# Optimization experiments

Measured on AMD Instinct MI355X. Metric: run time of the kernel, lower is better.

Reference implementation:

```python
import jax, jax.numpy as jnp
import numpy as np

TEMPERATURE = 0.01
STRIDE = 16  # original image coords -> feature grid (1024 / 64)


def setup_inputs() -> dict:
    key = jax.random.key(0)
    k1, k2, k3, k4, k5 = jax.random.split(key, 5)
    B, C, Hf, Wf, N = 32, 256, 64, 64, 64
    feats_src = jax.random.normal(k1, (B, C, Hf, Wf), dtype=jnp.float32)
    feats_trg = jax.random.normal(k2, (B, C, Hf, Wf), dtype=jnp.float32)
    # keypoints in original-image coordinates [0, 1024)
    kps_src = jax.random.uniform(k3, (B, N, 2), dtype=jnp.float32) * 1024.0
    kps_trg = jax.random.uniform(k4, (B, N, 2), dtype=jnp.float32) * 1024.0
    kps_mask = jax.random.bernoulli(k5, 0.7, (B, N))
    return {"feats_src": feats_src, "feats_trg": feats_trg,
            "kps_src": kps_src, "kps_trg": kps_trg, "kps_mask": kps_mask}


def _l2_normalize(x):
    # F.normalize(x, dim=1): x / max(||x||_2, eps)
    n = jnp.linalg.norm(x, axis=1, keepdims=True)
    return x / jnp.maximum(n, 1e-12)


def _kps_to_flat_idx(kps, Hf, Wf):
    # int(coord/16) truncation (coords >= 0 so trunc == floor), then clamp.
    fx = jnp.clip((kps[..., 0] / STRIDE).astype(jnp.int32), 0, Wf - 1)
    fy = jnp.clip((kps[..., 1] / STRIDE).astype(jnp.int32), 0, Hf - 1)
    return fy * Wf + fx  # (B, N)


def reference(feats_src, feats_trg, kps_src, kps_trg, kps_mask):
    B, C, Hf, Wf = feats_src.shape
    fs = _l2_normalize(feats_src).reshape(B, C, Hf * Wf)
    ft = _l2_normalize(feats_trg).reshape(B, C, Hf * Wf)

    src_idx = _kps_to_flat_idx(kps_src, Hf, Wf)  # (B, N)
    trg_idx = _kps_to_flat_idx(kps_trg, Hf, Wf)  # (B, N)

    # Gather query vectors at source keypoint cells: (B, C, N)
    queries = jnp.take_along_axis(fs, src_idx[:, None, :], axis=2)
    # Batched logits over all target cells: (B, N, Hf*Wf)
    logits = jnp.einsum('bcn,bcm->bnm', queries, ft) / TEMPERATURE

    logp = jax.nn.log_softmax(logits, axis=-1)
    nll = -jnp.take_along_axis(logp, trg_idx[..., None], axis=-1)[..., 0]  # (B, N)

    m = kps_mask.astype(nll.dtype)
    count = jnp.sum(m)
    # Masked mean over valid keypoints; 0 if no valid keypoints (matches torch).
    return jnp.sum(nll * m) / jnp.maximum(count, 1.0)
```

## Files before the change

### kernel.cpp

```cpp
#include <hip/hip_runtime.h>
#include <hip/hip_fp16.h>
#include <cstdint>

#define BB 32
#define CC 256
#define HF 64
#define WF 64
#define MM 4096
#define NN 64
#define MCHUNKS 32
#define MPB 128
#define KSTEPS 8

typedef _Float16 half8 __attribute__((ext_vector_type(8)));
typedef __fp16 fp16x2 __attribute__((ext_vector_type(2)));
typedef float f32x4 __attribute__((ext_vector_type(4)));


__global__ void phase0_gather_norm(const float* __restrict__ fs,
                                   const float* __restrict__ kps_src,
                                   const float* __restrict__ kps_trg,
                                   _Float16* __restrict__ wq,
                                   int* __restrict__ trgidx) {
  int blk = blockIdx.x;
  int b = blk >> 6, n = blk & 63;
  int c = threadIdx.x;

  float kx = kps_src[blk * 2 + 0];
  float ky = kps_src[blk * 2 + 1];
  int fx = min(max((int)(kx * (1.0f / 16.0f)), 0), WF - 1);
  int fy = min(max((int)(ky * (1.0f / 16.0f)), 0), HF - 1);
  int pix = fy * WF + fx;

  float x = fs[((size_t)b * CC + c) * MM + pix];

  float v = x * x;
  #pragma unroll
  for (int off = 32; off >= 1; off >>= 1) v += __shfl_xor(v, off);
  __shared__ float ssum[4];
  int wid = c >> 6, lane = c & 63;
  if (lane == 0) ssum[wid] = v;
  __syncthreads();
  float tot = ssum[0] + ssum[1] + ssum[2] + ssum[3];
  float inv = 1.0f / fmaxf(sqrtf(tot), 1e-12f);

  int ks = c >> 5, kg = (c >> 3) & 3, j = c & 7;
  int nt = n >> 4, nr = n & 15;
  int lane_f = kg * 16 + nr;
  size_t off = (size_t)b * 16384 + (size_t)((ks * 4 + nt) * 64 + lane_f) * 8 + j;
  wq[off] = (_Float16)(x * inv);

  if (c == 0) {
    float tx = kps_trg[blk * 2 + 0], ty = kps_trg[blk * 2 + 1];
    int gx = min(max((int)(tx * (1.0f / 16.0f)), 0), WF - 1);
    int gy = min(max((int)(ty * (1.0f / 16.0f)), 0), HF - 1);
    trgidx[blk] = gy * WF + gx;
  }
}

__global__ void __launch_bounds__(256, 4)
phaseB(const float* __restrict__ ft,
       const _Float16* __restrict__ wq,
       const int* __restrict__ tidx,
       float* __restrict__ part,
       float* __restrict__ trgl) {
  __shared__ _Float16 qf[16384];
  __shared__ int trg_lds[NN];
  __shared__ float pM[4 * NN], pS[4 * NN];

  int b = blockIdx.x >> 5, mc = blockIdx.x & 31;
  int tid = threadIdx.x;

  const uint4* src = (const uint4*)(wq + (size_t)b * 16384);
  uint4* dst = (uint4*)qf;
  #pragma unroll
  for (int i = 0; i < 8; ++i) dst[tid + 256 * i] = src[tid + 256 * i];
  if (tid < NN) trg_lds[tid] = tidx[b * NN + tid];
  __syncthreads();

  int w = tid >> 6, lane = tid & 63, g = lane >> 4, col = lane & 15;
  int m0 = mc * MPB + w * 32;
  const float* fb = ft + (size_t)b * CC * MM;
  const float* lb0 = fb + (size_t)(g * 8) * MM + (m0 + col);
  const float* lb1 = lb0 + 16;

  f32x4 acc[4][2];
  #pragma unroll
  for (int nt = 0; nt < 4; ++nt)
    #pragma unroll
    for (int mt = 0; mt < 2; ++mt) acc[nt][mt] = (f32x4){0.f, 0.f, 0.f, 0.f};
  float ss0 = 0.f, ss1 = 0.f;

  const half8* qv = (const half8*)qf;

  float cur0[8], cur1[8], nxt0[8], nxt1[8];
  #pragma unroll
  for (int j = 0; j < 8; ++j) {
    cur0[j] = lb0[(size_t)j * MM];
    cur1[j] = lb1[(size_t)j * MM];
  }

  #pragma unroll
  for (int ks = 0; ks < KSTEPS; ++ks) {
    if (ks + 1 < KSTEPS) {
      #pragma unroll
      for (int j = 0; j < 8; ++j) {
        nxt0[j] = lb0[(size_t)((ks + 1) * 32 + j) * MM];
        nxt1[j] = lb1[(size_t)((ks + 1) * 32 + j) * MM];
      }
    }

    half8 a0 = qv[(ks * 4 + 0) * 64 + lane];
    half8 a1 = qv[(ks * 4 + 1) * 64 + lane];
    half8 a2 = qv[(ks * 4 + 2) * 64 + lane];
    half8 a3 = qv[(ks * 4 + 3) * 64 + lane];

    half8 b0, b1;
    #pragma unroll
    for (int j = 0; j < 4; ++j) {
      ss0 += cur0[2 * j] * cur0[2 * j] + cur0[2 * j + 1] * cur0[2 * j + 1];
      ss1 += cur1[2 * j] * cur1[2 * j] + cur1[2 * j + 1] * cur1[2 * j + 1];
      fp16x2 h0 = __builtin_amdgcn_cvt_pkrtz(cur0[2 * j], cur0[2 * j + 1]);
      fp16x2 h1 = __builtin_amdgcn_cvt_pkrtz(cur1[2 * j], cur1[2 * j + 1]);
      b0[2 * j] = (_Float16)h0[0]; b0[2 * j + 1] = (_Float16)h0[1];
      b1[2 * j] = (_Float16)h1[0]; b1[2 * j + 1] = (_Float16)h1[1];
    }

    acc[0][0] = __builtin_amdgcn_mfma_f32_16x16x32_f16(a0, b0, acc[0][0], 0, 0, 0);
    acc[1][0] = __builtin_amdgcn_mfma_f32_16x16x32_f16(a1, b0, acc[1][0], 0, 0, 0);
    acc[2][0] = __builtin_amdgcn_mfma_f32_16x16x32_f16(a2, b0, acc[2][0], 0, 0, 0);
    acc[3][0] = __builtin_amdgcn_mfma_f32_16x16x32_f16(a3, b0, acc[3][0], 0, 0, 0);
    acc[0][1] = __builtin_amdgcn_mfma_f32_16x16x32_f16(a0, b1, acc[0][1], 0, 0, 0);
    acc[1][1] = __builtin_amdgcn_mfma_f32_16x16x32_f16(a1, b1, acc[1][1], 0, 0, 0);
    acc[2][1] = __builtin_amdgcn_mfma_f32_16x16x32_f16(a2, b1, acc[2][1], 0, 0, 0);
    acc[3][1] = __builtin_amdgcn_mfma_f32_16x16x32_f16(a3, b1, acc[3][1], 0, 0, 0);

    #pragma unroll
    for (int j = 0; j < 8; ++j) { cur0[j] = nxt0[j]; cur1[j] = nxt1[j]; }
  }

  ss0 += __shfl_xor(ss0, 16); ss0 += __shfl_xor(ss0, 32);
  ss1 += __shfl_xor(ss1, 16); ss1 += __shfl_xor(ss1, 32);
  float scale0 = 100.0f / fmaxf(sqrtf(ss0), 1e-12f);
  float scale1 = 100.0f / fmaxf(sqrtf(ss1), 1e-12f);

  int mA = m0 + col, mB = m0 + 16 + col;

  #pragma unroll
  for (int nt = 0; nt < 4; ++nt) {
    #pragma unroll
    for (int r = 0; r < 4; ++r) {
      int n = nt * 16 + g * 4 + r;
      float v0 = acc[nt][0][r] * scale0;
      float v1 = acc[nt][1][r] * scale1;
      int t = trg_lds[n];
      if (t == mA) trgl[b * NN + n] = v0;
      if (t == mB) trgl[b * NN + n] = v1;
      float mx = fmaxf(v0, v1);
      #pragma unroll
      for (int off = 8; off >= 1; off >>= 1) mx = fmaxf(mx, __shfl_xor(mx, off));
      float s = __expf(v0 - mx) + __expf(v1 - mx);
      #pragma unroll
      for (int off = 8; off >= 1; off >>= 1) s += __shfl_xor(s, off);
      if (col == 0) { pM[w * NN + n] = mx; pS[w * NN + n] = s; }
    }
  }
  __syncthreads();

  if (tid < NN) {
    int n = tid;
    float gm = fmaxf(fmaxf(pM[n], pM[NN + n]), fmaxf(pM[2 * NN + n], pM[3 * NN + n]));
    float S = 0.f;
    #pragma unroll
    for (int ww = 0; ww < 4; ++ww)
      S += pS[ww * NN + n] * __expf(pM[ww * NN + n] - gm);
    size_t o = ((size_t)mc * (BB * NN) + b * NN + n) * 2;
    part[o] = gm;
    part[o + 1] = S;
  }
}

__global__ void __launch_bounds__(1024)
reduceAB(const float* __restrict__ part,
         const float* __restrict__ trgl,
         const void* __restrict__ maskp,
         float* __restrict__ out) {
  int tid = threadIdx.x;

  __shared__ int flagF, flagB;
  if (tid == 0) { flagF = 0; flagB = 0; }
  __syncthreads();

  const unsigned char* mb = (const unsigned char*)maskp;
  int lf = 0, lb = 0;
  for (int i = tid; i < BB * NN; i += 1024) {
    unsigned char v = mb[i];
    int r = i & 3;
    if (r == 3 && v == 0x3F) lf = 1;
    if (r != 0 && v != 0) lb = 1;
  }
  if (lf) atomicOr(&flagF, 1);
  if (lb) atomicOr(&flagB, 1);
  __syncthreads();
  int layout = flagF ? 2 : (flagB ? 0 : 1);

  float lsum = 0.f, lcnt = 0.f;
  #pragma unroll
  for (int h = 0; h < 2; ++h) {
    int p = tid + h * 1024;
    float gm = -1e30f;
    #pragma unroll
    for (int c = 0; c < MCHUNKS; ++c)
      gm = fmaxf(gm, part[((size_t)c * (BB * NN) + p) * 2]);
    float S = 0.f;
    #pragma unroll
    for (int c = 0; c < MCHUNKS; ++c) {
      size_t o = ((size_t)c * (BB * NN) + p) * 2;
      S += part[o + 1] * __expf(part[o] - gm);
    }
    float nll = gm + logf(S) - trgl[p];

    float mval;
    if (layout == 2) mval = ((const float*)maskp)[p];
    else if (layout == 0) mval = (float)mb[p];
    else mval = (float)((const int*)maskp)[p];
    lsum += nll * mval;
    lcnt += mval;
  }

  #pragma unroll
  for (int off = 32; off >= 1; off >>= 1) {
    lsum += __shfl_xor(lsum, off);
    lcnt += __shfl_xor(lcnt, off);
  }
  __shared__ float sS[16], sC[16];
  int wid = tid >> 6, lane = tid & 63;
  if (lane == 0) { sS[wid] = lsum; sC[wid] = lcnt; }
  __syncthreads();
  if (tid == 0) {
    float s = 0.f, cn = 0.f;
    #pragma unroll
    for (int i = 0; i < 16; ++i) { s += sS[i]; cn += sC[i]; }
    out[0] = s / fmaxf(cn, 1.0f);
  }
}

extern "C" void kernel_launch(void* const* d_in, const int* in_sizes, int n_in,
                              void* d_out, int out_size, void* d_ws, size_t ws_size,
                              hipStream_t stream) {
  const float* fs   = (const float*)d_in[0];
  const float* ft   = (const float*)d_in[1];
  const float* ksrc = (const float*)d_in[2];
  const float* ktrg = (const float*)d_in[3];
  const void*  mask = d_in[4];
  float* out = (float*)d_out;

  _Float16* wq = (_Float16*)d_ws;
  float* part  = (float*)((char*)d_ws + (size_t)BB * 16384 * 2);
  float* trgl  = part + (size_t)MCHUNKS * BB * NN * 2;
  int* tidx    = (int*)(trgl + BB * NN);

  phase0_gather_norm<<<BB * NN, 256, 0, stream>>>(fs, ksrc, ktrg, wq, tidx);
  phaseB<<<BB * MCHUNKS, 256, 0, stream>>>(ft, wq, tidx, part, trgl);
  reduceAB<<<1, 1024, 0, stream>>>(part, trgl, mask, out);
}
```

Measured before the change: 58.08 us.

## Fuse final reduction into phaseB via last-block counter and transpose MFMA operands

Removes the separate reduceAB launch by having the last phaseB block, found through an atomic counter reset in phase0, perform the global log-sum-exp and masked mean. It also swaps the MFMA A/B operands so each lane holds per-keypoint columns, which lets the row max and sum reductions use two cross-group shuffles instead of four-step shuffles per row. Partial max and sum are split into separate arrays and merged with an online rescaling in the final block. The cost is a threadfence and atomic in every block, plus a serial tail reduction done by a single 256-thread block.

```diff
diff --git a/kernel.cpp b/kernel.cpp
--- a/kernel.cpp
+++ b/kernel.cpp
@@ -11,6 +11,7 @@
 #define MCHUNKS 32
 #define MPB 128
 #define KSTEPS 8
+#define NBLK (BB * MCHUNKS)
 
 typedef _Float16 half8 __attribute__((ext_vector_type(8)));
 typedef __fp16 fp16x2 __attribute__((ext_vector_type(2)));
@@ -21,10 +22,13 @@
                                    const float* __restrict__ kps_src,
                                    const float* __restrict__ kps_trg,
                                    _Float16* __restrict__ wq,
-                                   int* __restrict__ trgidx) {
+                                   int* __restrict__ trgidx,
+                                   int* __restrict__ counter) {
   int blk = blockIdx.x;
   int b = blk >> 6, n = blk & 63;
   int c = threadIdx.x;
+
+  if (blk == 0 && c == 0) *counter = 0;
 
   float kx = kps_src[blk * 2 + 0];
   float ky = kps_src[blk * 2 + 1];
@@ -58,15 +62,24 @@
   }
 }
 
+__device__ __forceinline__ float agent_load(const float* p) {
+  return __hip_atomic_load(p, __ATOMIC_RELAXED, __HIP_MEMORY_SCOPE_AGENT);
+}
+
 __global__ void __launch_bounds__(256, 4)
 phaseB(const float* __restrict__ ft,
        const _Float16* __restrict__ wq,
        const int* __restrict__ tidx,
-       float* __restrict__ part,
-       float* __restrict__ trgl) {
+       float* __restrict__ partM,
+       float* __restrict__ partS,
+       float* __restrict__ trgl,
+       const void* __restrict__ maskp,
+       float* __restrict__ out,
+       int* __restrict__ counter) {
   __shared__ _Float16 qf[16384];
   __shared__ int trg_lds[NN];
   __shared__ float pM[4 * NN], pS[4 * NN];
+  __shared__ int lastFlag;
 
   int b = blockIdx.x >> 5, mc = blockIdx.x & 31;
   int tid = threadIdx.x;
@@ -126,14 +139,14 @@
       b1[2 * j] = (_Float16)h1[0]; b1[2 * j + 1] = (_Float16)h1[1];
     }
 
-    acc[0][0] = __builtin_amdgcn_mfma_f32_16x16x32_f16(a0, b0, acc[0][0], 0, 0, 0);
-    acc[1][0] = __builtin_amdgcn_mfma_f32_16x16x32_f16(a1, b0, acc[1][0], 0, 0, 0);
-    acc[2][0] = __builtin_amdgcn_mfma_f32_16x16x32_f16(a2, b0, acc[2][0], 0, 0, 0);
-    acc[3][0] = __builtin_amdgcn_mfma_f32_16x16x32_f16(a3, b0, acc[3][0], 0, 0, 0);
-    acc[0][1] = __builtin_amdgcn_mfma_f32_16x16x32_f16(a0, b1, acc[0][1], 0, 0, 0);
-    acc[1][1] = __builtin_amdgcn_mfma_f32_16x16x32_f16(a1, b1, acc[1][1], 0, 0, 0);
-    acc[2][1] = __builtin_amdgcn_mfma_f32_16x16x32_f16(a2, b1, acc[2][1], 0, 0, 0);
-    acc[3][1] = __builtin_amdgcn_mfma_f32_16x16x32_f16(a3, b1, acc[3][1], 0, 0, 0);
+    acc[0][0] = __builtin_amdgcn_mfma_f32_16x16x32_f16(b0, a0, acc[0][0], 0, 0, 0);
+    acc[1][0] = __builtin_amdgcn_mfma_f32_16x16x32_f16(b0, a1, acc[1][0], 0, 0, 0);
+    acc[2][0] = __builtin_amdgcn_mfma_f32_16x16x32_f16(b0, a2, acc[2][0], 0, 0, 0);
+    acc[3][0] = __builtin_amdgcn_mfma_f32_16x16x32_f16(b0, a3, acc[3][0], 0, 0, 0);
+    acc[0][1] = __builtin_amdgcn_mfma_f32_16x16x32_f16(b1, a0, acc[0][1], 0, 0, 0);
+    acc[1][1] = __builtin_amdgcn_mfma_f32_16x16x32_f16(b1, a1, acc[1][1], 0, 0, 0);
+    acc[2][1] = __builtin_amdgcn_mfma_f32_16x16x32_f16(b1, a2, acc[2][1], 0, 0, 0);
+    acc[3][1] = __builtin_amdgcn_mfma_f32_16x16x32_f16(b1, a3, acc[3][1], 0, 0, 0);
 
     #pragma unroll
     for (int j = 0; j < 8; ++j) { cur0[j] = nxt0[j]; cur1[j] = nxt1[j]; }
@@ -141,29 +154,41 @@
 
   ss0 += __shfl_xor(ss0, 16); ss0 += __shfl_xor(ss0, 32);
   ss1 += __shfl_xor(ss1, 16); ss1 += __shfl_xor(ss1, 32);
-  float scale0 = 100.0f / fmaxf(sqrtf(ss0), 1e-12f);
-  float scale1 = 100.0f / fmaxf(sqrtf(ss1), 1e-12f);
-
-  int mA = m0 + col, mB = m0 + 16 + col;
+
+  float sc0[4], sc1[4];
+  #pragma unroll
+  for (int r = 0; r < 4; ++r) {
+    float t0 = __shfl(ss0, g * 4 + r, 16);
+    float t1 = __shfl(ss1, g * 4 + r, 16);
+    sc0[r] = 100.0f / fmaxf(sqrtf(t0), 1e-12f);
+    sc1[r] = 100.0f / fmaxf(sqrtf(t1), 1e-12f);
+  }
 
   #pragma unroll
   for (int nt = 0; nt < 4; ++nt) {
+    int n = nt * 16 + col;
+    int t = trg_lds[n];
+    float v[8];
     #pragma unroll
     for (int r = 0; r < 4; ++r) {
-      int n = nt * 16 + g * 4 + r;
-      float v0 = acc[nt][0][r] * scale0;
-      float v1 = acc[nt][1][r] * scale1;
-      int t = trg_lds[n];
-      if (t == mA) trgl[b * NN + n] = v0;
-      if (t == mB) trgl[b * NN + n] = v1;
-      float mx = fmaxf(v0, v1);
-      #pragma unroll
-      for (int off = 8; off >= 1; off >>= 1) mx = fmaxf(mx, __shfl_xor(mx, off));
-      float s = __expf(v0 - mx) + __expf(v1 - mx);
-      #pragma unroll
-      for (int off = 8; off >= 1; off >>= 1) s += __shfl_xor(s, off);
-      if (col == 0) { pM[w * NN + n] = mx; pS[w * NN + n] = s; }
-    }
+      v[r]     = acc[nt][0][r] * sc0[r];
+      v[4 + r] = acc[nt][1][r] * sc1[r];
+    }
+    #pragma unroll
+    for (int r = 0; r < 4; ++r) {
+      if (t == m0 + g * 4 + r)      trgl[b * NN + n] = v[r];
+      if (t == m0 + 16 + g * 4 + r) trgl[b * NN + n] = v[4 + r];
+    }
+    float mx = fmaxf(fmaxf(fmaxf(v[0], v[1]), fmaxf(v[2], v[3])),
+                     fmaxf(fmaxf(v[4], v[5]), fmaxf(v[6], v[7])));
+    mx = fmaxf(mx, __shfl_xor(mx, 16));
+    mx = fmaxf(mx, __shfl_xor(mx, 32));
+    float s = 0.f;
+    #pragma unroll
+    for (int j = 0; j < 8; ++j) s += __expf(v[j] - mx);
+    s += __shfl_xor(s, 16);
+    s += __shfl_xor(s, 32);
+    if (g == 0) { pM[w * NN + n] = mx; pS[w * NN + n] = s; }
   }
   __syncthreads();
 
@@ -174,30 +199,26 @@
     #pragma unroll
     for (int ww = 0; ww < 4; ++ww)
       S += pS[ww * NN + n] * __expf(pM[ww * NN + n] - gm);
-    size_t o = ((size_t)mc * (BB * NN) + b * NN + n) * 2;
-    part[o] = gm;
-    part[o + 1] = S;
-  }
-}
-
-__global__ void __launch_bounds__(1024)
-reduceAB(const float* __restrict__ part,
-         const float* __restrict__ trgl,
-         const void* __restrict__ maskp,
-         float* __restrict__ out) {
-  int tid = threadIdx.x;
+    partM[mc * (BB * NN) + b * NN + n] = gm;
+    partS[mc * (BB * NN) + b * NN + n] = S;
+  }
+
+  __threadfence();
+  if (tid == 0) lastFlag = (atomicAdd(counter, 1) == NBLK - 1) ? 1 : 0;
+  __syncthreads();
+  if (!lastFlag) return;
+  __threadfence();
 
   __shared__ int flagF, flagB;
   if (tid == 0) { flagF = 0; flagB = 0; }
   __syncthreads();
-
   const unsigned char* mb = (const unsigned char*)maskp;
   int lf = 0, lb = 0;
-  for (int i = tid; i < BB * NN; i += 1024) {
-    unsigned char v = mb[i];
+  for (int i = tid; i < BB * NN; i += 256) {
+    unsigned char vch = mb[i];
     int r = i & 3;
-    if (r == 3 && v == 0x3F) lf = 1;
-    if (r != 0 && v != 0) lb = 1;
+    if (r == 3 && vch == 0x3F) lf = 1;
+    if (r != 0 && vch != 0) lb = 1;
   }
   if (lf) atomicOr(&flagF, 1);
   if (lb) atomicOr(&flagB, 1);
@@ -206,19 +227,17 @@
 
   float lsum = 0.f, lcnt = 0.f;
   #pragma unroll
-  for (int h = 0; h < 2; ++h) {
-    int p = tid + h * 1024;
-    float gm = -1e30f;
-    #pragma unroll
-    for (int c = 0; c < MCHUNKS; ++c)
-      gm = fmaxf(gm, part[((size_t)c * (BB * NN) + p) * 2]);
-    float S = 0.f;
-    #pragma unroll
-    for (int c = 0; c < MCHUNKS; ++c) {
-      size_t o = ((size_t)c * (BB * NN) + p) * 2;
-      S += part[o + 1] * __expf(part[o] - gm);
-    }
-    float nll = gm + logf(S) - trgl[p];
+  for (int h = 0; h < 8; ++h) {
+    int p = tid + h * 256;
+    float gm = -1e30f, S = 0.f;
+    for (int c2 = 0; c2 < MCHUNKS; ++c2) {
+      float mi = agent_load(&partM[c2 * (BB * NN) + p]);
+      float si = agent_load(&partS[c2 * (BB * NN) + p]);
+      float nm = fmaxf(gm, mi);
+      S = S * __expf(gm - nm) + si * __expf(mi - nm);
+      gm = nm;
+    }
+    float nll = gm + logf(S) - agent_load(&trgl[p]);
 
     float mval;
     if (layout == 2) mval = ((const float*)maskp)[p];
@@ -233,14 +252,13 @@
     lsum += __shfl_xor(lsum, off);
     lcnt += __shfl_xor(lcnt, off);
   }
-  __shared__ float sS[16], sC[16];
-  int wid = tid >> 6, lane = tid & 63;
-  if (lane == 0) { sS[wid] = lsum; sC[wid] = lcnt; }
+  __shared__ float sS[4], sC[4];
+  int wid2 = tid >> 6, lane2 = tid & 63;
+  if (lane2 == 0) { sS[wid2] = lsum; sC[wid2] = lcnt; }
   __syncthreads();
   if (tid == 0) {
-    float s = 0.f, cn = 0.f;
-    #pragma unroll
-    for (int i = 0; i < 16; ++i) { s += sS[i]; cn += sC[i]; }
+    float s = sS[0] + sS[1] + sS[2] + sS[3];
+    float cn = sC[0] + sC[1] + sC[2] + sC[3];
     out[0] = s / fmaxf(cn, 1.0f);
   }
 }
@@ -256,11 +274,12 @@
   float* out = (float*)d_out;
 
   _Float16* wq = (_Float16*)d_ws;
-  float* part  = (float*)((char*)d_ws + (size_t)BB * 16384 * 2);
-  float* trgl  = part + (size_t)MCHUNKS * BB * NN * 2;
+  float* partM = (float*)((char*)d_ws + (size_t)BB * 16384 * 2);
+  float* partS = partM + (size_t)MCHUNKS * BB * NN;
+  float* trgl  = partS + (size_t)MCHUNKS * BB * NN;
   int* tidx    = (int*)(trgl + BB * NN);
-
-  phase0_gather_norm<<<BB * NN, 256, 0, stream>>>(fs, ksrc, ktrg, wq, tidx);
-  phaseB<<<BB * MCHUNKS, 256, 0, stream>>>(ft, wq, tidx, part, trgl);
-  reduceAB<<<1, 1024, 0, stream>>>(part, trgl, mask, out);
-}
+  int* counter = tidx + BB * NN;
+
+  phase0_gather_norm<<<BB * NN, 256, 0, stream>>>(fs, ksrc, ktrg, wq, tidx, counter);
+  phaseB<<<NBLK, 256, 0, stream>>>(ft, wq, tidx, partM, partS, trgl, mask, out, counter);
+}
```

After: 181.5 us. 213% more time.
